# Optimization experiments

Hardware: AMD Instinct MI355X
Metric: run time of the kernel (lower is better)

The kernel has to match this reference:

```python
import jax, jax.numpy as jnp
import numpy as np

N_TOTAL = 524288  # total entity embeddings in flat ragged buffer
A = 262144        # number of actors
D = 256           # d_model
C = 32            # n_choice


def setup_inputs() -> dict:
    key = jax.random.key(0)
    k1, k2, k3, k4, k5 = jax.random.split(key, 5)
    x_data = jax.random.normal(k1, (N_TOTAL, D), dtype=jnp.float32)
    W = jax.random.normal(k2, (C, D), dtype=jnp.float32) * 0.01  # layer_init std=0.01
    b = jnp.zeros((C,), dtype=jnp.float32)
    actors = jax.random.randint(k3, (A,), 0, N_TOTAL, dtype=jnp.int64)
    mask = jax.random.randint(k4, (A, C), 0, 2, dtype=jnp.int32)
    mask = mask.at[:, 0].set(1)  # guarantee at least one valid choice per actor
    pa = jax.random.randint(k5, (A,), 0, C, dtype=jnp.int64)
    # prev_actions must be valid under the mask (as a real rollout would be)
    valid = jnp.take_along_axis(mask, pa[:, None], axis=1).squeeze(-1)
    prev_actions = jnp.where(valid != 0, pa, 0)
    return {"x_data": x_data, "W": W, "b": b, "actors": actors,
            "mask": mask, "prev_actions": prev_actions}


def reference(x_data, W, b, actors, mask, prev_actions):
    # gather actor embeddings: [A, D]
    actor_embeds = x_data[actors]
    # linear projection: [A, C]
    logits = jnp.einsum('ad,cd->ac', actor_embeds, W) + b
    # masked fill with -inf where mask == 0
    logits = jnp.where(mask == 0, -jnp.inf, logits)
    # Categorical: normalized logits = log_softmax
    logp = jax.nn.log_softmax(logits, axis=-1)
    p = jnp.exp(logp)
    action = prev_actions  # prev_actions provided -> no sampling
    logprob = jnp.take_along_axis(logp, action[:, None], axis=1).squeeze(-1)
    # entropy: -sum p*logp over valid entries (0*(-inf) -> 0)
    entropy = -jnp.sum(jnp.where(mask != 0, p * logp, 0.0), axis=-1)
    return action, logprob, entropy, logp
```

## Files before the change

### kernel.cpp

```cpp
#include <hip/hip_runtime.h>
#include <math.h>


constexpr int A_TOTAL = 262144;
constexpr int DMODEL  = 256;
constexpr int NCHOICE = 32;
constexpr int APW     = 32;
constexpr int PADC    = 36;

#define MASK_NEG 1.0e30f

#define DPP_SUM_STEP(x, ctrl)                                              \
    (x) += __int_as_float(__builtin_amdgcn_update_dpp(                     \
        0, __float_as_int(x), (ctrl), 0xf, 0xf, true))
#define DPP_MAX_STEP(x, ctrl)                                              \
    (x) = fmaxf((x), __int_as_float(__builtin_amdgcn_update_dpp(           \
        0, __float_as_int(x), (ctrl), 0xf, 0xf, true)))

#define DPP_REDUCE_DG(x)                                                   \
    do { DPP_SUM_STEP(x, 0xB1); DPP_SUM_STEP(x, 0x4E);                     \
         DPP_SUM_STEP(x, 0x128); DPP_SUM_STEP(x, 0x124); } while (0)
#define DPP_RED8_SUM(x)                                                    \
    do { DPP_SUM_STEP(x, 0xB1); DPP_SUM_STEP(x, 0x4E);                     \
         DPP_SUM_STEP(x, 0x141); } while (0)
#define DPP_RED8_MAX(x)                                                    \
    do { DPP_MAX_STEP(x, 0xB1); DPP_MAX_STEP(x, 0x4E);                     \
         DPP_MAX_STEP(x, 0x141); } while (0)

__global__ __launch_bounds__(64, 2)
void cat_action_head(const float* __restrict__ x_data,
                     const float* __restrict__ W,
                     const float* __restrict__ bvec,
                     const int*   __restrict__ actors,
                     const int*   __restrict__ mask,
                     const int*   __restrict__ prev_actions,
                     float* __restrict__ out)
{
    const int ln = threadIdx.x & 63;
    const int dg = ln & 15;
    const int cg = ln >> 4;
    const int q  = ln & 7;
    const int ar = ln >> 3;

    float* out_action  = out;
    float* out_logprob = out + A_TOTAL;
    float* out_entropy = out + 2 * A_TOTAL;
    float* out_logp    = out + 3 * A_TOTAL;

    __shared__ float part[8][PADC];

    const int wbase = blockIdx.x * APW;

    int sa[APW];
#pragma unroll
    for (int v = 0; v < APW / 4; ++v) {
        const int4 av = *reinterpret_cast<const int4*>(&actors[wbase + v * 4]);
        sa[v * 4 + 0] = __builtin_amdgcn_readfirstlane(av.x);
        sa[v * 4 + 1] = __builtin_amdgcn_readfirstlane(av.y);
        sa[v * 4 + 2] = __builtin_amdgcn_readfirstlane(av.z);
        sa[v * 4 + 3] = __builtin_amdgcn_readfirstlane(av.w);
    }

    float4 Wf[8][4];
#pragma unroll
    for (int k = 0; k < 8; ++k) {
        const float* Wr = W + (size_t)(cg * 8 + k) * DMODEL + dg * 4;
#pragma unroll
        for (int j = 0; j < 4; ++j)
            Wf[k][j] = *reinterpret_cast<const float4*>(Wr + j * 64);
    }

    const float4 bq = *reinterpret_cast<const float4*>(&bvec[q * 4]);

    int4 mvC = *reinterpret_cast<const int4*>(
                   &mask[(size_t)(wbase + ar) * NCHOICE + q * 4]);
    int  pvC = prev_actions[wbase + ar];

#define LOADX(DST, I)                                                      \
    do {                                                                   \
        const float* xb_ = x_data + (size_t)sa[(I)] * DMODEL + dg * 4;     \
        DST[0] = *reinterpret_cast<const float4*>(xb_);                    \
        DST[1] = *reinterpret_cast<const float4*>(xb_ + 64);               \
        DST[2] = *reinterpret_cast<const float4*>(xb_ + 128);              \
        DST[3] = *reinterpret_cast<const float4*>(xb_ + 192);              \
    } while (0)

#define COMP(XV, II)                                                       \
    do {                                                                   \
        float acc_[8] = {0.f,0.f,0.f,0.f,0.f,0.f,0.f,0.f};                 \
        _Pragma("unroll")                                                  \
        for (int j = 0; j < 4; ++j) {                                      \
            _Pragma("unroll")                                              \
            for (int k2 = 0; k2 < 8; ++k2) {                               \
                acc_[k2] = fmaf(XV[j].x, Wf[k2][j].x, acc_[k2]);           \
                acc_[k2] = fmaf(XV[j].y, Wf[k2][j].y, acc_[k2]);           \
                acc_[k2] = fmaf(XV[j].z, Wf[k2][j].z, acc_[k2]);           \
                acc_[k2] = fmaf(XV[j].w, Wf[k2][j].w, acc_[k2]);           \
            }                                                              \
        }                                                                  \
        _Pragma("unroll")                                                  \
        for (int k2 = 0; k2 < 8; ++k2) DPP_REDUCE_DG(acc_[k2]);            \
        if (dg == 0) {                                                     \
            float4 v0_; v0_.x=acc_[0]; v0_.y=acc_[1];                      \
                        v0_.z=acc_[2]; v0_.w=acc_[3];                      \
            float4 v1_; v1_.x=acc_[4]; v1_.y=acc_[5];                      \
                        v1_.z=acc_[6]; v1_.w=acc_[7];                      \
            *reinterpret_cast<float4*>(&part[II][cg * 8])     = v0_;       \
            *reinterpret_cast<float4*>(&part[II][cg * 8 + 4]) = v1_;       \
        }                                                                  \
    } while (0)

#define EPI(K, MV, PV)                                                     \
    do {                                                                   \
        const int aep_ = wbase + (K) * 8 + ar;                             \
        const float4 pv4_ =                                                \
            *reinterpret_cast<const float4*>(&part[ar][q * 4]);            \
        const float lg0 = (MV).x ? pv4_.x + bq.x : -MASK_NEG;              \
        const float lg1 = (MV).y ? pv4_.y + bq.y : -MASK_NEG;              \
        const float lg2 = (MV).z ? pv4_.z + bq.z : -MASK_NEG;              \
        const float lg3 = (MV).w ? pv4_.w + bq.w : -MASK_NEG;              \
        float mx = fmaxf(fmaxf(lg0, lg1), fmaxf(lg2, lg3));                \
        DPP_RED8_MAX(mx);                                                  \
        const float e0 = expf(lg0 - mx);                                   \
        const float e1 = expf(lg1 - mx);                                   \
        const float e2 = expf(lg2 - mx);                                   \
        const float e3 = expf(lg3 - mx);                                   \
        float se = (e0 + e1) + (e2 + e3);                                  \
        DPP_RED8_SUM(se);                                                  \
        const float lse = mx + logf(se);                                   \
        const float rse = 1.0f / se;                                       \
        const float lp0 = lg0 - lse;                                       \
        const float lp1 = lg1 - lse;                                       \
        const float lp2 = lg2 - lse;                                       \
        const float lp3 = lg3 - lse;                                       \
        float4 lpv; lpv.x=lp0; lpv.y=lp1; lpv.z=lp2; lpv.w=lp3;            \
        *reinterpret_cast<float4*>(                                        \
            &out_logp[(size_t)aep_ * NCHOICE + q * 4]) = lpv;              \
        float ent = fmaf(e0, lp0, fmaf(e1, lp1, fmaf(e2, lp2, e3 * lp3))); \
        DPP_RED8_SUM(ent);                                                 \
        float sel = ((PV) == q * 4 + 0) ? lp0 : 0.0f;                      \
        sel = ((PV) == q * 4 + 1) ? lp1 : sel;                             \
        sel = ((PV) == q * 4 + 2) ? lp2 : sel;                             \
        sel = ((PV) == q * 4 + 3) ? lp3 : sel;                             \
        DPP_RED8_SUM(sel);                                                 \
        if (q == 0) {                                                      \
            out_logprob[aep_] = sel;                                       \
            out_entropy[aep_] = -ent * rse;                                \
            out_action[aep_]  = (float)(PV);                               \
        }                                                                  \
    } while (0)

#define PFM(G)                                                             \
    do {                                                                   \
        mvC = *reinterpret_cast<const int4*>(                              \
            &mask[(size_t)(wbase + (G) * 8 + ar) * NCHOICE + q * 4]);      \
        pvC = prev_actions[wbase + (G) * 8 + ar];                          \
    } while (0)

#define STEP(I, B)                                                         \
    do {                                                                   \
        COMP(B, (I) & 7);                                                  \
        if ((I) + 4 < APW) LOADX(B, (I) + 4);                              \
    } while (0)

    float4 X0[4], X1[4], X2[4], X3[4];
    LOADX(X0, 0); LOADX(X1, 1); LOADX(X2, 2); LOADX(X3, 3);

    STEP(0, X0);  STEP(1, X1);  STEP(2, X2);  STEP(3, X3);
    STEP(4, X0);  STEP(5, X1);  STEP(6, X2);  STEP(7, X3);
    EPI(0, mvC, pvC); PFM(1);
    STEP(8, X0);  STEP(9, X1);  STEP(10, X2); STEP(11, X3);
    STEP(12, X0); STEP(13, X1); STEP(14, X2); STEP(15, X3);
    EPI(1, mvC, pvC); PFM(2);
    STEP(16, X0); STEP(17, X1); STEP(18, X2); STEP(19, X3);
    STEP(20, X0); STEP(21, X1); STEP(22, X2); STEP(23, X3);
    EPI(2, mvC, pvC); PFM(3);
    STEP(24, X0); STEP(25, X1); STEP(26, X2); STEP(27, X3);
    STEP(28, X0); STEP(29, X1); STEP(30, X2); STEP(31, X3);
    EPI(3, mvC, pvC);

#undef STEP
#undef PFM
#undef EPI
#undef COMP
#undef LOADX
}

extern "C" void kernel_launch(void* const* d_in, const int* in_sizes, int n_in,
                              void* d_out, int out_size, void* d_ws, size_t ws_size,
                              hipStream_t stream)
{
    const float* x_data = (const float*)d_in[0];
    const float* W      = (const float*)d_in[1];
    const float* bvec   = (const float*)d_in[2];
    const int*   actors = (const int*)d_in[3];
    const int*   mask   = (const int*)d_in[4];
    const int*   prev   = (const int*)d_in[5];
    float*       o      = (float*)d_out;

    const int nblocks = A_TOTAL / APW;
    cat_action_head<<<nblocks, 64, 0, stream>>>(x_data, W, bvec, actors, mask,
                                                prev, o);
}
```

Before: 90.48 us.

## Split choices across two waves per block with shared-memory exchange and barriers

```diff
diff --git a/kernel.cpp b/kernel.cpp
--- a/kernel.cpp
+++ b/kernel.cpp
@@ -5,7 +5,7 @@
 constexpr int A_TOTAL = 262144;
 constexpr int DMODEL  = 256;
 constexpr int NCHOICE = 32;
-constexpr int APW     = 32;
+constexpr int APB     = 32;
 constexpr int PADC    = 36;
 
 #define MASK_NEG 1.0e30f
@@ -27,7 +27,11 @@
     do { DPP_MAX_STEP(x, 0xB1); DPP_MAX_STEP(x, 0x4E);                     \
          DPP_MAX_STEP(x, 0x141); } while (0)
 
-__global__ __launch_bounds__(64, 2)
+#define RAW_BARRIER()                                                      \
+    do { asm volatile("s_waitcnt lgkmcnt(0)" ::: "memory");                \
+         asm volatile("s_barrier" ::: "memory"); } while (0)
+
+__global__ __launch_bounds__(128, 4)
 void cat_action_head(const float* __restrict__ x_data,
                      const float* __restrict__ W,
                      const float* __restrict__ bvec,
@@ -36,24 +40,25 @@
                      const int*   __restrict__ prev_actions,
                      float* __restrict__ out)
 {
-    const int ln = threadIdx.x & 63;
-    const int dg = ln & 15;
-    const int cg = ln >> 4;
-    const int q  = ln & 7;
-    const int ar = ln >> 3;
+    const int ln  = threadIdx.x & 63;
+    const int h   = threadIdx.x >> 6;
+    const int dg  = ln & 15;
+    const int cg4 = ln >> 4;
+    const int q   = ln & 7;
+    const int ar4 = (ln >> 3) & 3;
 
     float* out_action  = out;
     float* out_logprob = out + A_TOTAL;
     float* out_entropy = out + 2 * A_TOTAL;
     float* out_logp    = out + 3 * A_TOTAL;
 
-    __shared__ float part[8][PADC];
-
-    const int wbase = blockIdx.x * APW;
-
-    int sa[APW];
+    __shared__ float part[2][8][PADC];
+
+    const int wbase = blockIdx.x * APB;
+
+    int sa[APB];
 #pragma unroll
-    for (int v = 0; v < APW / 4; ++v) {
+    for (int v = 0; v < APB / 4; ++v) {
         const int4 av = *reinterpret_cast<const int4*>(&actors[wbase + v * 4]);
         sa[v * 4 + 0] = __builtin_amdgcn_readfirstlane(av.x);
         sa[v * 4 + 1] = __builtin_amdgcn_readfirstlane(av.y);
@@ -61,10 +66,10 @@
         sa[v * 4 + 3] = __builtin_amdgcn_readfirstlane(av.w);
     }
 
-    float4 Wf[8][4];
+    float4 Wf[4][4];
 #pragma unroll
-    for (int k = 0; k < 8; ++k) {
-        const float* Wr = W + (size_t)(cg * 8 + k) * DMODEL + dg * 4;
+    for (int k = 0; k < 4; ++k) {
+        const float* Wr = W + (size_t)(h * 16 + cg4 * 4 + k) * DMODEL + dg * 4;
 #pragma unroll
         for (int j = 0; j < 4; ++j)
             Wf[k][j] = *reinterpret_cast<const float4*>(Wr + j * 64);
@@ -73,8 +78,8 @@
     const float4 bq = *reinterpret_cast<const float4*>(&bvec[q * 4]);
 
     int4 mvC = *reinterpret_cast<const int4*>(
-                   &mask[(size_t)(wbase + ar) * NCHOICE + q * 4]);
-    int  pvC = prev_actions[wbase + ar];
+                   &mask[(size_t)(wbase + h * 4 + ar4) * NCHOICE + q * 4]);
+    int  pvC = prev_actions[wbase + h * 4 + ar4];
 
 #define LOADX(DST, I)                                                      \
     do {                                                                   \
@@ -85,36 +90,42 @@
         DST[3] = *reinterpret_cast<const float4*>(xb_ + 192);              \
     } while (0)
 
-#define COMP(XV, II)                                                       \
-    do {                                                                   \
-        float acc_[8] = {0.f,0.f,0.f,0.f,0.f,0.f,0.f,0.f};                 \
+#define COMP(XV, G, II)                                                    \
+    do {                                                                   \
+        float a0_ = 0.f, a1_ = 0.f, a2_ = 0.f, a3_ = 0.f;                  \
         _Pragma("unroll")                                                  \
         for (int j = 0; j < 4; ++j) {                                      \
-            _Pragma("unroll")                                              \
-            for (int k2 = 0; k2 < 8; ++k2) {                               \
-                acc_[k2] = fmaf(XV[j].x, Wf[k2][j].x, acc_[k2]);           \
-                acc_[k2] = fmaf(XV[j].y, Wf[k2][j].y, acc_[k2]);           \
-                acc_[k2] = fmaf(XV[j].z, Wf[k2][j].z, acc_[k2]);           \
-                acc_[k2] = fmaf(XV[j].w, Wf[k2][j].w, acc_[k2]);           \
-            }                                                              \
+            a0_ = fmaf(XV[j].x, Wf[0][j].x, a0_);                          \
+            a0_ = fmaf(XV[j].y, Wf[0][j].y, a0_);                          \
+            a0_ = fmaf(XV[j].z, Wf[0][j].z, a0_);                          \
+            a0_ = fmaf(XV[j].w, Wf[0][j].w, a0_);                          \
+            a1_ = fmaf(XV[j].x, Wf[1][j].x, a1_);                          \
+            a1_ = fmaf(XV[j].y, Wf[1][j].y, a1_);                          \
+            a1_ = fmaf(XV[j].z, Wf[1][j].z, a1_);                          \
+            a1_ = fmaf(XV[j].w, Wf[1][j].w, a1_);                          \
+            a2_ = fmaf(XV[j].x, Wf[2][j].x, a2_);                          \
+            a2_ = fmaf(XV[j].y, Wf[2][j].y, a2_);                          \
+            a2_ = fmaf(XV[j].z, Wf[2][j].z, a2_);                          \
+            a2_ = fmaf(XV[j].w, Wf[2][j].w, a2_);                          \
+            a3_ = fmaf(XV[j].x, Wf[3][j].x, a3_);                          \
+            a3_ = fmaf(XV[j].y, Wf[3][j].y, a3_);                          \
+            a3_ = fmaf(XV[j].z, Wf[3][j].z, a3_);                          \
+            a3_ = fmaf(XV[j].w, Wf[3][j].w, a3_);                          \
         }                                                                  \
-        _Pragma("unroll")                                                  \
-        for (int k2 = 0; k2 < 8; ++k2) DPP_REDUCE_DG(acc_[k2]);            \
+        DPP_REDUCE_DG(a0_); DPP_REDUCE_DG(a1_);                            \
+        DPP_REDUCE_DG(a2_); DPP_REDUCE_DG(a3_);                            \
         if (dg == 0) {                                                     \
-            float4 v0_; v0_.x=acc_[0]; v0_.y=acc_[1];                      \
-                        v0_.z=acc_[2]; v0_.w=acc_[3];                      \
-            float4 v1_; v1_.x=acc_[4]; v1_.y=acc_[5];                      \
-                        v1_.z=acc_[6]; v1_.w=acc_[7];                      \
-            *reinterpret_cast<float4*>(&part[II][cg * 8])     = v0_;       \
-            *reinterpret_cast<float4*>(&part[II][cg * 8 + 4]) = v1_;       \
+            float4 v_; v_.x = a0_; v_.y = a1_; v_.z = a2_; v_.w = a3_;     \
+            *reinterpret_cast<float4*>(                                    \
+                &part[(G) & 1][II][h * 16 + cg4 * 4]) = v_;                \
         }                                                                  \
     } while (0)
 
-#define EPI(K, MV, PV)                                                     \
-    do {                                                                   \
-        const int aep_ = wbase + (K) * 8 + ar;                             \
-        const float4 pv4_ =                                                \
-            *reinterpret_cast<const float4*>(&part[ar][q * 4]);            \
+#define EPI(G, MV, PV)                                                     \
+    do {                                                                   \
+        const int aep_ = wbase + (G) * 8 + h * 4 + ar4;                    \
+        const float4 pv4_ = *reinterpret_cast<const float4*>(              \
+            &part[(G) & 1][h * 4 + ar4][q * 4]);                           \
         const float lg0 = (MV).x ? pv4_.x + bq.x : -MASK_NEG;              \
         const float lg1 = (MV).y ? pv4_.y + bq.y : -MASK_NEG;              \
         const float lg2 = (MV).z ? pv4_.z + bq.z : -MASK_NEG;              \
@@ -133,9 +144,6 @@
         const float lp1 = lg1 - lse;                                       \
         const float lp2 = lg2 - lse;                                       \
         const float lp3 = lg3 - lse;                                       \
-        float4 lpv; lpv.x=lp0; lpv.y=lp1; lpv.z=lp2; lpv.w=lp3;            \
-        *reinterpret_cast<float4*>(                                        \
-            &out_logp[(size_t)aep_ * NCHOICE + q * 4]) = lpv;              \
         float ent = fmaf(e0, lp0, fmaf(e1, lp1, fmaf(e2, lp2, e3 * lp3))); \
         DPP_RED8_SUM(ent);                                                 \
         float sel = ((PV) == q * 4 + 0) ? lp0 : 0.0f;                      \
@@ -143,40 +151,51 @@
         sel = ((PV) == q * 4 + 2) ? lp2 : sel;                             \
         sel = ((PV) == q * 4 + 3) ? lp3 : sel;                             \
         DPP_RED8_SUM(sel);                                                 \
-        if (q == 0) {                                                      \
-            out_logprob[aep_] = sel;                                       \
-            out_entropy[aep_] = -ent * rse;                                \
-            out_action[aep_]  = (float)(PV);                               \
+        if (threadIdx.x == (unsigned)(h * 64 + (threadIdx.x & 63)) &&      \
+            (threadIdx.x & 63) < 32) {                                     \
+            float4 lpv; lpv.x=lp0; lpv.y=lp1; lpv.z=lp2; lpv.w=lp3;        \
+            *reinterpret_cast<float4*>(                                    \
+                &out_logp[(size_t)aep_ * NCHOICE + q * 4]) = lpv;          \
+            if (q == 0) {                                                  \
+                out_logprob[aep_] = sel;                                   \
+                out_entropy[aep_] = -ent * rse;                            \
+                out_action[aep_]  = (float)(PV);                           \
+            }                                                              \
         }                                                                  \
     } while (0)
 
 #define PFM(G)                                                             \
     do {                                                                   \
         mvC = *reinterpret_cast<const int4*>(                              \
-            &mask[(size_t)(wbase + (G) * 8 + ar) * NCHOICE + q * 4]);      \
-        pvC = prev_actions[wbase + (G) * 8 + ar];                          \
+            &mask[(size_t)(wbase + (G) * 8 + h * 4 + ar4) * NCHOICE        \
+                  + q * 4]);                                               \
+        pvC = prev_actions[wbase + (G) * 8 + h * 4 + ar4];                 \
     } while (0)
 
 #define STEP(I, B)                                                         \
     do {                                                                   \
-        COMP(B, (I) & 7);                                                  \
-        if ((I) + 4 < APW) LOADX(B, (I) + 4);                              \
-    } while (0)
-
-    float4 X0[4], X1[4], X2[4], X3[4];
-    LOADX(X0, 0); LOADX(X1, 1); LOADX(X2, 2); LOADX(X3, 3);
-
-    STEP(0, X0);  STEP(1, X1);  STEP(2, X2);  STEP(3, X3);
-    STEP(4, X0);  STEP(5, X1);  STEP(6, X2);  STEP(7, X3);
+        COMP(B, (I) >> 3, (I) & 7);                                        \
+        if ((I) + 2 < APB) LOADX(B, (I) + 2);                              \
+    } while (0)
+
+    float4 X0[4], X1[4];
+    LOADX(X0, 0); LOADX(X1, 1);
+
+    STEP(0, X0);  STEP(1, X1);  STEP(2, X0);  STEP(3, X1);
+    STEP(4, X0);  STEP(5, X1);  STEP(6, X0);  STEP(7, X1);
+    RAW_BARRIER();
     EPI(0, mvC, pvC); PFM(1);
-    STEP(8, X0);  STEP(9, X1);  STEP(10, X2); STEP(11, X3);
-    STEP(12, X0); STEP(13, X1); STEP(14, X2); STEP(15, X3);
+    STEP(8, X0);  STEP(9, X1);  STEP(10, X0); STEP(11, X1);
+    STEP(12, X0); STEP(13, X1); STEP(14, X0); STEP(15, X1);
+    RAW_BARRIER();
     EPI(1, mvC, pvC); PFM(2);
-    STEP(16, X0); STEP(17, X1); STEP(18, X2); STEP(19, X3);
-    STEP(20, X0); STEP(21, X1); STEP(22, X2); STEP(23, X3);
+    STEP(16, X0); STEP(17, X1); STEP(18, X0); STEP(19, X1);
+    STEP(20, X0); STEP(21, X1); STEP(22, X0); STEP(23, X1);
+    RAW_BARRIER();
     EPI(2, mvC, pvC); PFM(3);
-    STEP(24, X0); STEP(25, X1); STEP(26, X2); STEP(27, X3);
-    STEP(28, X0); STEP(29, X1); STEP(30, X2); STEP(31, X3);
+    STEP(24, X0); STEP(25, X1); STEP(26, X0); STEP(27, X1);
+    STEP(28, X0); STEP(29, X1); STEP(30, X0); STEP(31, X1);
+    RAW_BARRIER();
     EPI(3, mvC, pvC);
 
 #undef STEP
@@ -198,7 +217,7 @@
     const int*   prev   = (const int*)d_in[5];
     float*       o      = (float*)d_out;
 
-    const int nblocks = A_TOTAL / APW;
-    cat_action_head<<<nblocks, 64, 0, stream>>>(x_data, W, bvec, actors, mask,
-                                                prev, o);
+    const int nblocks = A_TOTAL / APB;
+    cat_action_head<<<nblocks, 128, 0, stream>>>(x_data, W, bvec, actors, mask,
+                                                 prev, o);
 }
```

Result: slower. 136.4 us (+50.7%).
